# Performance work log

Hardware: AMD Instinct MI355X
Metric: run time of the kernel (lower is better)

Reference implementation:

```python
import jax, jax.numpy as jnp
import numpy as np

B, N, D = 8, 2048, 512
H = 8
DH = D // H          # 64
SR = 2               # sr_ratio
EPS = 1e-5


def setup_inputs() -> dict:
    key = jax.random.key(0)
    ks = jax.random.split(key, 10)
    s = 0.02
    return {
        "x": jax.random.normal(ks[0], (B, N, D), jnp.float32),
        "x_kv": jax.random.normal(ks[1], (B, N, D), jnp.float32),
        "Wq": jax.random.normal(ks[2], (D, D), jnp.float32) * s,
        "bq": jnp.zeros((D,), jnp.float32),
        "Wsr": jax.random.normal(ks[3], (D, D, SR), jnp.float32) * s,  # (out_ch, in_ch, kernel)
        "bsr": jnp.zeros((D,), jnp.float32),
        "gamma": jnp.ones((D,), jnp.float32),
        "beta": jnp.zeros((D,), jnp.float32),
        "Wkv": jax.random.normal(ks[4], (D, 2 * D), jnp.float32) * s,
        "bkv": jnp.zeros((2 * D,), jnp.float32),
        "Wp": jax.random.normal(ks[5], (DH, DH), jnp.float32) * s,
        "bp": jnp.zeros((DH,), jnp.float32),
    }


def reference(x, x_kv, Wq, bq, Wsr, bsr, gamma, beta, Wkv, bkv, Wp, bp):
    b, n, d = x.shape
    # query projection -> (B, N, H, DH)
    q = (x @ Wq + bq).reshape(b, n, H, DH)

    # spatial reduction: Conv1d(kernel=stride=SR) over sequence, then LayerNorm
    # non-overlapping windows -> reshape + einsum
    xk = x_kv.reshape(b, -1, SR, d)                      # (B, Nk/SR, SR, D)
    xk = jnp.einsum('btsi,ois->bto', xk, Wsr) + bsr       # (B, Nk_eff, D)
    mu = xk.mean(-1, keepdims=True)
    var = jnp.mean((xk - mu) ** 2, -1, keepdims=True)
    xk = (xk - mu) * jax.lax.rsqrt(var + EPS) * gamma + beta

    # kv projection: (B, Nk, 2, H, DH) -> (2, B, H, Nk, DH)
    nk = xk.shape[1]
    kv = (xk @ Wkv + bkv).reshape(b, nk, 2, H, DH)
    kv = jnp.transpose(kv, (2, 0, 3, 1, 4))
    k, v = kv[0], kv[1]                                   # (B, H, Nk, DH)

    # faithful reproduction of original permutes/views
    q = jnp.transpose(q, (2, 0, 1, 3)).reshape(b * H, n, DH)      # (H,B,N,d)->(BH,N,d)
    k = jnp.transpose(k, (2, 0, 1, 3)).reshape(b * H, nk, DH)     # (Nk,B,H,d)->(BH,Nk,d)
    v = jnp.transpose(v, (2, 0, 1, 3)).reshape(b * H, nk, DH)

    scale = float(np.sqrt(DH))
    score = jnp.einsum('bnd,bmd->bnm', q, k) / scale
    attn = jax.nn.softmax(score, axis=-1)
    ctx = jnp.einsum('bnm,bmd->bnd', attn, v)
    ctx = ctx @ Wp + bp                                   # per-head proj Linear(DH, DH)

    ctx = ctx.reshape(H, b, n, DH)
    ctx = jnp.transpose(ctx, (1, 2, 0, 3)).reshape(b, n, H * DH)
    return ctx, attn
```

## Files before the change

kernel.cpp:

```cpp
#include <hip/hip_runtime.h>
#include <cstdint>

using f32x4 = __attribute__((ext_vector_type(4))) float;
using s16x8 = __attribute__((ext_vector_type(8))) short;
using s16x4 = __attribute__((ext_vector_type(4))) short;

__device__ __forceinline__ short f2bf(float f) {
    union { float f; uint32_t u; } x{f};
    uint32_t r = (x.u + 0x7fffu + ((x.u >> 16) & 1u)) >> 16;
    return (short)r;
}
__device__ __forceinline__ float bf2f(short s) {
    union { uint32_t u; float f; } x;
    x.u = ((uint32_t)(uint16_t)s) << 16;
    return x.f;
}

#define MFMA16(a, b, c) __builtin_amdgcn_mfma_f32_16x16x32_bf16(a, b, c, 0, 0, 0)

__device__ __forceinline__ void bar_lgkm() {
    asm volatile("s_waitcnt lgkmcnt(0)\n\ts_barrier" ::: "memory");
}

__device__ __forceinline__ void gl_lds16(const void* g, void* l) {
    __builtin_amdgcn_global_load_lds(
        (const __attribute__((address_space(1))) void*)(const void*)g,
        (__attribute__((address_space(3))) void*)l, 16, 0, 0);
}

__global__ __launch_bounds__(256) void cvt_bf16_2(
    const float* __restrict__ a, const float* __restrict__ b,
    short* __restrict__ oa, short* __restrict__ ob)
{
    size_t i = ((size_t)blockIdx.x * 256 + threadIdx.x) * 8;
    float4 va0 = *(const float4*)(a + i), va1 = *(const float4*)(a + i + 4);
    float4 vb0 = *(const float4*)(b + i), vb1 = *(const float4*)(b + i + 4);
    s16x8 ra, rb;
    ra[0]=f2bf(va0.x); ra[1]=f2bf(va0.y); ra[2]=f2bf(va0.z); ra[3]=f2bf(va0.w);
    ra[4]=f2bf(va1.x); ra[5]=f2bf(va1.y); ra[6]=f2bf(va1.z); ra[7]=f2bf(va1.w);
    rb[0]=f2bf(vb0.x); rb[1]=f2bf(vb0.y); rb[2]=f2bf(vb0.z); rb[3]=f2bf(vb0.w);
    rb[4]=f2bf(vb1.x); rb[5]=f2bf(vb1.y); rb[6]=f2bf(vb1.z); rb[7]=f2bf(vb1.w);
    *(s16x8*)(oa + i) = ra;
    *(s16x8*)(ob + i) = rb;
}

__global__ __launch_bounds__(256) void prep_w(
    const float* __restrict__ Wq, const float* __restrict__ Wsr,
    const float* __restrict__ Wkv, const float* __restrict__ Wp,
    short* __restrict__ WqT, short* __restrict__ W2T,
    short* __restrict__ WkvT, short* __restrict__ WpT)
{
    int t = blockIdx.x * 256 + threadIdx.x;
    if (t < 262144) {
        int o = t >> 9, k = t & 511;
        WqT[t] = f2bf(Wq[k * 512 + o]);
    } else if (t < 786432) {
        int u = t - 262144;
        int o = u >> 10, kk = u & 1023;
        int s = kk >> 9, i = kk & 511;
        W2T[u] = f2bf(Wsr[o * 1024 + i * 2 + s]);
    } else if (t < 1310720) {
        int u = t - 786432;
        int c = u >> 9, k = u & 511;
        WkvT[u] = f2bf(Wkv[k * 1024 + c]);
    } else if (t < 1314816) {
        int u = t - 1310720;
        int e = u >> 6, dh = u & 63;
        WpT[u] = f2bf(Wp[dh * 64 + e]);
    }
}

__global__ __launch_bounds__(256) void ln_kernel(
    const float* __restrict__ xkf, const float* __restrict__ gamma,
    const float* __restrict__ beta, short* __restrict__ out)
{
    int row = blockIdx.x * 4 + (threadIdx.x >> 6);
    int lane = threadIdx.x & 63;
    const float* p = xkf + (size_t)row * 512 + lane * 8;
    float4 v0 = *(const float4*)p, v1 = *(const float4*)(p + 4);
    float vv[8] = {v0.x, v0.y, v0.z, v0.w, v1.x, v1.y, v1.z, v1.w};
    float s = 0.f, q = 0.f;
#pragma unroll
    for (int j = 0; j < 8; ++j) { s += vv[j]; q += vv[j] * vv[j]; }
#pragma unroll
    for (int m = 1; m < 64; m <<= 1) { s += __shfl_xor(s, m); q += __shfl_xor(q, m); }
    float mean = s * (1.f / 512.f);
    float var  = q * (1.f / 512.f) - mean * mean;
    float rstd = rsqrtf(var + 1e-5f);
    s16x8 o;
#pragma unroll
    for (int j = 0; j < 8; ++j)
        o[j] = f2bf((vv[j] - mean) * rstd * gamma[lane * 8 + j] + beta[lane * 8 + j]);
    *(s16x8*)(out + (size_t)row * 512 + lane * 8) = o;
}

template <int EPI>
__global__ __launch_bounds__(256) void gemm_bt(
    const short* __restrict__ A, const short* __restrict__ BT,
    const float* __restrict__ bias,
    float* __restrict__ outF, short* __restrict__ outS, short* __restrict__ outS2,
    int M, int N, int K)
{
    __shared__ short As[128 * 32];
    __shared__ short Bs[128 * 32];
    const int tid = threadIdx.x;
    const int wv = tid >> 6, lane = tid & 63;
    const int l15 = lane & 15, lhi = lane >> 4;
    const int wr = wv >> 1, wc = wv & 1;
    const int m0 = blockIdx.y * 128, n0 = blockIdx.x * 128;

    f32x4 acc[4][4] = {};

    const int nk = K >> 5;
    for (int kk = 0; kk < nk; ++kk) {
#pragma unroll
        for (int i = 0; i < 2; ++i) {
            int fo = wv * 2048 + i * 1024 + lane * 16;
            int row = fo >> 6;
            int ks  = (fo & 63) >> 1;
            gl_lds16(A  + (size_t)(m0 + row) * K + kk * 32 + ks, (char*)As + fo);
            gl_lds16(BT + (size_t)(n0 + row) * K + kk * 32 + ks, (char*)Bs + fo);
        }
        __syncthreads();
        s16x8 a[4], b[4];
#pragma unroll
        for (int mi = 0; mi < 4; ++mi)
            a[mi] = *(const s16x8*)&As[(wr * 64 + mi * 16 + l15) * 32 + lhi * 8];
#pragma unroll
        for (int ni = 0; ni < 4; ++ni)
            b[ni] = *(const s16x8*)&Bs[(wc * 64 + ni * 16 + l15) * 32 + lhi * 8];
#pragma unroll
        for (int mi = 0; mi < 4; ++mi)
#pragma unroll
            for (int ni = 0; ni < 4; ++ni)
                acc[mi][ni] = MFMA16(a[mi], b[ni], acc[mi][ni]);
        __syncthreads();
    }

#pragma unroll
    for (int mi = 0; mi < 4; ++mi) {
#pragma unroll
        for (int ni = 0; ni < 4; ++ni) {
#pragma unroll
            for (int r = 0; r < 4; ++r) {
                int grow = m0 + wr * 64 + mi * 16 + lhi * 4 + r;
                int gcol = n0 + wc * 64 + ni * 16 + l15;
                float v = acc[mi][ni][r] + bias[gcol];
                if constexpr (EPI == 0) {
                    int h = gcol >> 6, dh = gcol & 63;
                    int bb = grow >> 11, n = grow & 2047;
                    outS[(((size_t)(h * 8 + bb) * 2048 + n) << 6) + dh] = f2bf(v * 0.125f);
                } else if constexpr (EPI == 1) {
                    outF[(size_t)grow * 512 + gcol] = v;
                } else {
                    int kvsel = gcol >> 9, h = (gcol >> 6) & 7, dh = gcol & 63;
                    int bb = grow >> 10, t = grow & 1023;
                    int g2 = t >> 4, m = ((t & 15) << 6) + bb * 8 + h;
                    if (kvsel == 0)
                        outS[(((size_t)g2 * 1024 + m) << 6) + dh] = f2bf(v);
                    else
                        outS2[(((size_t)g2 * 64 + dh) << 10) + m] = f2bf(v);
                }
            }
        }
    }
}

__global__ __launch_bounds__(512, 4) void attn_kernel(
    const short* __restrict__ Qb, const short* __restrict__ Kb,
    const short* __restrict__ VTb, const short* __restrict__ WpT,
    const float* __restrict__ bp,
    float* __restrict__ ctx_out, float* __restrict__ attn_out)
{
    __shared__ __align__(16) char smem[65536];
    __shared__ float sums[8][32];

    const int bid = blockIdx.x;
    const int swz = ((bid & 7) << 9) | (bid >> 3);
    const int g  = swz >> 6;
    const int n0 = (swz & 63) << 5;
    const int tid = threadIdx.x;
    const int wv = tid >> 6, lane = tid & 63;
    const int l15 = lane & 15, lhi = lane >> 4;

    s16x8 qa00, qa01, qa10, qa11;
    {
        size_t qb0 = (((size_t)g * 2048 + n0 + l15) << 6) + lhi * 8;
        size_t qb1 = (((size_t)g * 2048 + n0 + 16 + l15) << 6) + lhi * 8;
        qa00 = *(const s16x8*)&Qb[qb0];
        qa01 = *(const s16x8*)&Qb[qb0 + 32];
        qa10 = *(const s16x8*)&Qb[qb1];
        qa11 = *(const s16x8*)&Qb[qb1 + 32];
    }

    const short* Kg = Kb + ((size_t)g << 16);
    float ps0[4] = {}, ps1[4] = {};
#pragma unroll 2
    for (int i = 0; i < 8; ++i) {
        int mf = wv * 8 + i;
        const short* kr = Kg + ((mf * 16 + l15) << 6) + lhi * 8;
        s16x8 k0 = *(const s16x8*)kr;
        s16x8 k1 = *(const s16x8*)(kr + 32);
        f32x4 s0 = {0.f, 0.f, 0.f, 0.f};
        s0 = MFMA16(qa00, k0, s0);
        s0 = MFMA16(qa01, k1, s0);
        f32x4 s1 = {0.f, 0.f, 0.f, 0.f};
        s1 = MFMA16(qa10, k0, s1);
        s1 = MFMA16(qa11, k1, s1);
#pragma unroll
        for (int r = 0; r < 4; ++r) {
            float e0 = __expf(s0[r]);
            ps0[r] += e0;
            int row0 = lhi * 4 + r;
            int byte0 = ((row0 << 11) + ((mf * 16 + l15) << 1)) ^ ((row0 & 7) << 4);
            *(short*)(smem + byte0) = f2bf(e0);
            float e1 = __expf(s1[r]);
            ps1[r] += e1;
            int row1 = 16 + lhi * 4 + r;
            int byte1 = ((row1 << 11) + ((mf * 16 + l15) << 1)) ^ ((row1 & 7) << 4);
            *(short*)(smem + byte1) = f2bf(e1);
        }
    }
#pragma unroll
    for (int r = 0; r < 4; ++r) {
        float v0 = ps0[r], v1 = ps1[r];
        v0 += __shfl_xor(v0, 1); v1 += __shfl_xor(v1, 1);
        v0 += __shfl_xor(v0, 2); v1 += __shfl_xor(v1, 2);
        v0 += __shfl_xor(v0, 4); v1 += __shfl_xor(v1, 4);
        v0 += __shfl_xor(v0, 8); v1 += __shfl_xor(v1, 8);
        ps0[r] = v0; ps1[r] = v1;
    }
    if (l15 == 0) {
#pragma unroll
        for (int r = 0; r < 4; ++r) {
            sums[wv][lhi * 4 + r] = ps0[r];
            sums[wv][16 + lhi * 4 + r] = ps1[r];
        }
    }
    bar_lgkm();

    f32x4 ctx0[4] = {}, ctx1[4] = {};
    const short* Vg = VTb + ((size_t)g << 16);
#pragma unroll
    for (int kk = 0; kk < 4; ++kk) {
        int col = wv * 128 + kk * 32 + lhi * 8;
        int b0 = ((l15 << 11) + (col << 1)) ^ ((l15 & 7) << 4);
        int b1 = (((16 + l15) << 11) + (col << 1)) ^ ((l15 & 7) << 4);
        s16x8 pf0 = *(const s16x8*)(smem + b0);
        s16x8 pf1 = *(const s16x8*)(smem + b1);
#pragma unroll
        for (int ni = 0; ni < 4; ++ni) {
            s16x8 vb = *(const s16x8*)&Vg[((ni * 16 + l15) << 10) + col];
            ctx0[ni] = MFMA16(pf0, vb, ctx0[ni]);
            ctx1[ni] = MFMA16(pf1, vb, ctx1[ni]);
        }
    }
    __builtin_amdgcn_sched_barrier(0);

#pragma unroll
    for (int rr = 0; rr < 4; ++rr) {
        int row = wv * 4 + rr;
        float tot = 0.f;
#pragma unroll
        for (int w = 0; w < 8; ++w) tot += sums[w][row];
        float inv = 1.f / tot;
        float* arow = attn_out + (((size_t)g * 2048 + n0 + row) << 10);
#pragma unroll
        for (int it = 0; it < 2; ++it) {
            int col = it * 512 + lane * 8;
            int byte = ((row << 11) + (col << 1)) ^ ((row & 7) << 4);
            s16x8 p = *(const s16x8*)(smem + byte);
            f32x4 w0 = {bf2f(p[0]) * inv, bf2f(p[1]) * inv, bf2f(p[2]) * inv, bf2f(p[3]) * inv};
            f32x4 w1 = {bf2f(p[4]) * inv, bf2f(p[5]) * inv, bf2f(p[6]) * inv, bf2f(p[7]) * inv};
            __builtin_nontemporal_store(w0, (f32x4*)(arow + col));
            __builtin_nontemporal_store(w1, (f32x4*)(arow + col + 4));
        }
    }

    bar_lgkm();
    float* cx = (float*)smem;
    if (wv >= 4) {
        int q = wv - 4;
#pragma unroll
        for (int ni = 0; ni < 4; ++ni)
#pragma unroll
            for (int r = 0; r < 4; ++r) {
                cx[(q * 32 + lhi * 4 + r) * 68 + ni * 16 + l15] = ctx0[ni][r];
                cx[(q * 32 + 16 + lhi * 4 + r) * 68 + ni * 16 + l15] = ctx1[ni][r];
            }
    }
    bar_lgkm();
    if (wv < 4) {
#pragma unroll
        for (int ni = 0; ni < 4; ++ni)
#pragma unroll
            for (int r = 0; r < 4; ++r) {
                cx[(wv * 32 + lhi * 4 + r) * 68 + ni * 16 + l15] += ctx0[ni][r];
                cx[(wv * 32 + 16 + lhi * 4 + r) * 68 + ni * 16 + l15] += ctx1[ni][r];
            }
    }
    bar_lgkm();

    if (wv < 2) {
        int rbase = wv * 16;
        float tot = 0.f;
#pragma unroll
        for (int w = 0; w < 8; ++w) tot += sums[w][rbase + l15];
        float invq = 1.f / tot;
        s16x8 ca[2];
#pragma unroll
        for (int kk = 0; kk < 2; ++kk)
#pragma unroll
            for (int j = 0; j < 8; ++j) {
                int k = kk * 32 + lhi * 8 + j;
                int ri = (rbase + l15) * 68 + k;
                float v = cx[ri] + cx[2176 + ri] + cx[4352 + ri] + cx[6528 + ri];
                ca[kk][j] = f2bf(v * invq);
            }
        f32x4 acc2[4] = {};
#pragma unroll
        for (int ni = 0; ni < 4; ++ni) {
            s16x8 b0 = *(const s16x8*)&WpT[((ni * 16 + l15) << 6) + lhi * 8];
            s16x8 b1 = *(const s16x8*)&WpT[((ni * 16 + l15) << 6) + 32 + lhi * 8];
            acc2[ni] = MFMA16(ca[0], b0, acc2[ni]);
            acc2[ni] = MFMA16(ca[1], b1, acc2[ni]);
        }
        const int hh = g >> 3, bb = g & 7;
#pragma unroll
        for (int ni = 0; ni < 4; ++ni)
#pragma unroll
            for (int r = 0; r < 4; ++r) {
                int n = n0 + rbase + lhi * 4 + r;
                int e2 = ni * 16 + l15;
                ctx_out[((size_t)bb * 2048 + n) * 512 + hh * 64 + e2] = acc2[ni][r] + bp[e2];
            }
    }
}

extern "C" void kernel_launch(void* const* d_in, const int* in_sizes, int n_in,
                              void* d_out, int out_size, void* d_ws, size_t ws_size,
                              hipStream_t stream)
{
    const float* x     = (const float*)d_in[0];
    const float* xkv   = (const float*)d_in[1];
    const float* Wq    = (const float*)d_in[2];
    const float* bq    = (const float*)d_in[3];
    const float* Wsr   = (const float*)d_in[4];
    const float* bsr   = (const float*)d_in[5];
    const float* gamma = (const float*)d_in[6];
    const float* beta  = (const float*)d_in[7];
    const float* Wkv   = (const float*)d_in[8];
    const float* bkv   = (const float*)d_in[9];
    const float* Wp    = (const float*)d_in[10];
    const float* bp    = (const float*)d_in[11];

    float* ctx_out  = (float*)d_out;
    float* attn_out = ctx_out + (size_t)8 * 2048 * 512;

    char* sc = (char*)attn_out;
    short* xb   = (short*)sc;  sc += (size_t)16384 * 512 * 2;
    short* xkvb = (short*)sc;  sc += (size_t)8192 * 1024 * 2;
    float* xkf  = (float*)sc;  sc += (size_t)8192 * 512 * 4;
    short* xkln = (short*)sc;  sc += (size_t)8192 * 512 * 2;
    short* WqT  = (short*)sc;  sc += (size_t)512 * 512 * 2;
    short* W2T  = (short*)sc;  sc += (size_t)512 * 1024 * 2;
    short* WkvT = (short*)sc;  sc += (size_t)1024 * 512 * 2;

    char* ws = (char*)d_ws;
    short* Qb  = (short*)ws;   ws += (size_t)64 * 2048 * 64 * 2;
    short* Kb  = (short*)ws;   ws += (size_t)64 * 1024 * 64 * 2;
    short* VTb = (short*)ws;   ws += (size_t)64 * 64 * 1024 * 2;
    short* WpT = (short*)ws;   ws += (size_t)64 * 64 * 2;

    cvt_bf16_2<<<4096, 256, 0, stream>>>(x, xkv, xb, xkvb);
    prep_w<<<5136, 256, 0, stream>>>(Wq, Wsr, Wkv, Wp, WqT, W2T, WkvT, WpT);
    gemm_bt<0><<<dim3(4, 128), 256, 0, stream>>>(xb, WqT, bq, nullptr, Qb, nullptr, 16384, 512, 512);
    gemm_bt<1><<<dim3(4, 64), 256, 0, stream>>>(xkvb, W2T, bsr, xkf, nullptr, nullptr, 8192, 512, 1024);
    ln_kernel<<<2048, 256, 0, stream>>>(xkf, gamma, beta, xkln);
    gemm_bt<2><<<dim3(8, 64), 256, 0, stream>>>(xkln, WkvT, bkv, nullptr, Kb, VTb, 8192, 1024, 512);
    attn_kernel<<<4096, 512, 0, stream>>>(Qb, Kb, VTb, WpT, bp, ctx_out, attn_out);
}
```

Measured before the change: 335.7 us.

## Fuse fp32-to-bf16 input conversion into GEMM loads and prefetch K/V in attention

Removes the separate conversion kernel and instead has the Q and spatial-reduction GEMMs load fp32 activations, convert them to bf16 in registers and write them to LDS. This avoids a full write and re-read of bf16 copies of x and x_kv. In exchange, the A-tile loads become synchronous register round trips rather than direct global-to-LDS loads, and the GEMMs read twice the bytes for A. Separately, the attention kernel prefetches K and V fragments into registers a few iterations ahead to hide global load latency, at the cost of higher register pressure.

```diff
diff --git a/kernel.cpp b/kernel.cpp
--- a/kernel.cpp
+++ b/kernel.cpp
@@ -3,7 +3,6 @@
 
 using f32x4 = __attribute__((ext_vector_type(4))) float;
 using s16x8 = __attribute__((ext_vector_type(8))) short;
-using s16x4 = __attribute__((ext_vector_type(4))) short;
 
 __device__ __forceinline__ short f2bf(float f) {
     union { float f; uint32_t u; } x{f};
@@ -26,22 +25,6 @@
     __builtin_amdgcn_global_load_lds(
         (const __attribute__((address_space(1))) void*)(const void*)g,
         (__attribute__((address_space(3))) void*)l, 16, 0, 0);
-}
-
-__global__ __launch_bounds__(256) void cvt_bf16_2(
-    const float* __restrict__ a, const float* __restrict__ b,
-    short* __restrict__ oa, short* __restrict__ ob)
-{
-    size_t i = ((size_t)blockIdx.x * 256 + threadIdx.x) * 8;
-    float4 va0 = *(const float4*)(a + i), va1 = *(const float4*)(a + i + 4);
-    float4 vb0 = *(const float4*)(b + i), vb1 = *(const float4*)(b + i + 4);
-    s16x8 ra, rb;
-    ra[0]=f2bf(va0.x); ra[1]=f2bf(va0.y); ra[2]=f2bf(va0.z); ra[3]=f2bf(va0.w);
-    ra[4]=f2bf(va1.x); ra[5]=f2bf(va1.y); ra[6]=f2bf(va1.z); ra[7]=f2bf(va1.w);
-    rb[0]=f2bf(vb0.x); rb[1]=f2bf(vb0.y); rb[2]=f2bf(vb0.z); rb[3]=f2bf(vb0.w);
-    rb[4]=f2bf(vb1.x); rb[5]=f2bf(vb1.y); rb[6]=f2bf(vb1.z); rb[7]=f2bf(vb1.w);
-    *(s16x8*)(oa + i) = ra;
-    *(s16x8*)(ob + i) = rb;
 }
 
 __global__ __launch_bounds__(256) void prep_w(
@@ -94,9 +77,9 @@
     *(s16x8*)(out + (size_t)row * 512 + lane * 8) = o;
 }
 
-template <int EPI>
+template <int EPI, int AF32>
 __global__ __launch_bounds__(256) void gemm_bt(
-    const short* __restrict__ A, const short* __restrict__ BT,
+    const void* __restrict__ Ap, const short* __restrict__ BT,
     const float* __restrict__ bias,
     float* __restrict__ outF, short* __restrict__ outS, short* __restrict__ outS2,
     int M, int N, int K)
@@ -118,7 +101,17 @@
             int fo = wv * 2048 + i * 1024 + lane * 16;
             int row = fo >> 6;
             int ks  = (fo & 63) >> 1;
-            gl_lds16(A  + (size_t)(m0 + row) * K + kk * 32 + ks, (char*)As + fo);
+            if constexpr (AF32) {
+                const float* src = (const float*)Ap + (size_t)(m0 + row) * K + kk * 32 + ks;
+                float4 a0 = *(const float4*)src;
+                float4 a1 = *(const float4*)(src + 4);
+                s16x8 pk;
+                pk[0] = f2bf(a0.x); pk[1] = f2bf(a0.y); pk[2] = f2bf(a0.z); pk[3] = f2bf(a0.w);
+                pk[4] = f2bf(a1.x); pk[5] = f2bf(a1.y); pk[6] = f2bf(a1.z); pk[7] = f2bf(a1.w);
+                *(s16x8*)((char*)As + fo) = pk;
+            } else {
+                gl_lds16((const short*)Ap + (size_t)(m0 + row) * K + kk * 32 + ks, (char*)As + fo);
+            }
             gl_lds16(BT + (size_t)(n0 + row) * K + kk * 32 + ks, (char*)Bs + fo);
         }
         __syncthreads();
@@ -194,13 +187,23 @@
     }
 
     const short* Kg = Kb + ((size_t)g << 16);
+    s16x8 kf[4][2];
+#pragma unroll
+    for (int p = 0; p < 4; ++p) {
+        const short* kr = Kg + (((wv * 8 + p) * 16 + l15) << 6) + lhi * 8;
+        kf[p][0] = *(const s16x8*)kr;
+        kf[p][1] = *(const s16x8*)(kr + 32);
+    }
     float ps0[4] = {}, ps1[4] = {};
-#pragma unroll 2
+#pragma unroll
     for (int i = 0; i < 8; ++i) {
+        s16x8 k0 = kf[i & 3][0], k1 = kf[i & 3][1];
+        if (i < 4) {
+            const short* kr = Kg + (((wv * 8 + i + 4) * 16 + l15) << 6) + lhi * 8;
+            kf[i][0] = *(const s16x8*)kr;
+            kf[i][1] = *(const s16x8*)(kr + 32);
+        }
         int mf = wv * 8 + i;
-        const short* kr = Kg + ((mf * 16 + l15) << 6) + lhi * 8;
-        s16x8 k0 = *(const s16x8*)kr;
-        s16x8 k1 = *(const s16x8*)(kr + 32);
         f32x4 s0 = {0.f, 0.f, 0.f, 0.f};
         s0 = MFMA16(qa00, k0, s0);
         s0 = MFMA16(qa01, k1, s0);
@@ -221,6 +224,15 @@
             *(short*)(smem + byte1) = f2bf(e1);
         }
     }
+
+    const short* Vg = VTb + ((size_t)g << 16);
+    s16x8 vb[2][4];
+#pragma unroll
+    for (int ni = 0; ni < 4; ++ni) {
+        vb[0][ni] = *(const s16x8*)&Vg[((ni * 16 + l15) << 10) + wv * 128 + lhi * 8];
+        vb[1][ni] = *(const s16x8*)&Vg[((ni * 16 + l15) << 10) + wv * 128 + 32 + lhi * 8];
+    }
+
 #pragma unroll
     for (int r = 0; r < 4; ++r) {
         float v0 = ps0[r], v1 = ps1[r];
@@ -240,19 +252,26 @@
     bar_lgkm();
 
     f32x4 ctx0[4] = {}, ctx1[4] = {};
-    const short* Vg = VTb + ((size_t)g << 16);
 #pragma unroll
     for (int kk = 0; kk < 4; ++kk) {
         int col = wv * 128 + kk * 32 + lhi * 8;
+        s16x8 pv[4];
+#pragma unroll
+        for (int ni = 0; ni < 4; ++ni) pv[ni] = vb[kk & 1][ni];
+        if (kk < 2) {
+            int ncol = wv * 128 + (kk + 2) * 32 + lhi * 8;
+#pragma unroll
+            for (int ni = 0; ni < 4; ++ni)
+                vb[kk][ni] = *(const s16x8*)&Vg[((ni * 16 + l15) << 10) + ncol];
+        }
         int b0 = ((l15 << 11) + (col << 1)) ^ ((l15 & 7) << 4);
         int b1 = (((16 + l15) << 11) + (col << 1)) ^ ((l15 & 7) << 4);
         s16x8 pf0 = *(const s16x8*)(smem + b0);
         s16x8 pf1 = *(const s16x8*)(smem + b1);
 #pragma unroll
         for (int ni = 0; ni < 4; ++ni) {
-            s16x8 vb = *(const s16x8*)&Vg[((ni * 16 + l15) << 10) + col];
-            ctx0[ni] = MFMA16(pf0, vb, ctx0[ni]);
-            ctx1[ni] = MFMA16(pf1, vb, ctx1[ni]);
+            ctx0[ni] = MFMA16(pf0, pv[ni], ctx0[ni]);
+            ctx1[ni] = MFMA16(pf1, pv[ni], ctx1[ni]);
         }
     }
     __builtin_amdgcn_sched_barrier(0);
@@ -358,8 +377,6 @@
     float* attn_out = ctx_out + (size_t)8 * 2048 * 512;
 
     char* sc = (char*)attn_out;
-    short* xb   = (short*)sc;  sc += (size_t)16384 * 512 * 2;
-    short* xkvb = (short*)sc;  sc += (size_t)8192 * 1024 * 2;
     float* xkf  = (float*)sc;  sc += (size_t)8192 * 512 * 4;
     short* xkln = (short*)sc;  sc += (size_t)8192 * 512 * 2;
     short* WqT  = (short*)sc;  sc += (size_t)512 * 512 * 2;
@@ -372,11 +389,10 @@
     short* VTb = (short*)ws;   ws += (size_t)64 * 64 * 1024 * 2;
     short* WpT = (short*)ws;   ws += (size_t)64 * 64 * 2;
 
-    cvt_bf16_2<<<4096, 256, 0, stream>>>(x, xkv, xb, xkvb);
     prep_w<<<5136, 256, 0, stream>>>(Wq, Wsr, Wkv, Wp, WqT, W2T, WkvT, WpT);
-    gemm_bt<0><<<dim3(4, 128), 256, 0, stream>>>(xb, WqT, bq, nullptr, Qb, nullptr, 16384, 512, 512);
-    gemm_bt<1><<<dim3(4, 64), 256, 0, stream>>>(xkvb, W2T, bsr, xkf, nullptr, nullptr, 8192, 512, 1024);
+    gemm_bt<0, 1><<<dim3(4, 128), 256, 0, stream>>>(x, WqT, bq, nullptr, Qb, nullptr, 16384, 512, 512);
+    gemm_bt<1, 1><<<dim3(4, 64), 256, 0, stream>>>(xkv, W2T, bsr, xkf, nullptr, nullptr, 8192, 512, 1024);
     ln_kernel<<<2048, 256, 0, stream>>>(xkf, gamma, beta, xkln);
-    gemm_bt<2><<<dim3(8, 64), 256, 0, stream>>>(xkln, WkvT, bkv, nullptr, Kb, VTb, 8192, 1024, 512);
+    gemm_bt<2, 0><<<dim3(8, 64), 256, 0, stream>>>(xkln, WkvT, bkv, nullptr, Kb, VTb, 8192, 1024, 512);
     attn_kernel<<<4096, 512, 0, stream>>>(Qb, Kb, VTb, WpT, bp, ctx_out, attn_out);
 }
```

After: 329.5 us. Within noise of the previous version (-1.9%).
